# Optimization experiments

Measured on AMD Instinct MI355X. Metric: run time of the kernel, lower is better.

Reference implementation:

```python
import jax, jax.numpy as jnp
import numpy as np

NUM_HEADS = 8
OUT_DIM = 128
DEPTH = OUT_DIM // NUM_HEADS  # 16


def setup_inputs() -> dict:
    key = jax.random.key(0)
    ks = jax.random.split(key, 6)
    B, N, F_IN = 32, 512, 64
    x = jax.random.normal(ks[0], (B, N, F_IN), dtype=jnp.float32)
    adj = jax.random.uniform(ks[1], (B, N, N), dtype=jnp.float32)
    wq = jax.random.normal(ks[2], (F_IN, OUT_DIM), dtype=jnp.float32) * 0.05
    wk = jax.random.normal(ks[3], (F_IN, OUT_DIM), dtype=jnp.float32) * 0.05
    wv = jax.random.normal(ks[4], (F_IN, OUT_DIM), dtype=jnp.float32) * 0.05
    wo = jax.random.normal(ks[5], (OUT_DIM, OUT_DIM), dtype=jnp.float32) * 0.05
    return {"x": x, "adj": adj, "wq": wq, "wk": wk, "wv": wv, "wo": wo}


def _split_heads(t, B, N):
    # [B, N, out_dim] -> [B, H, N, D]
    return t.reshape(B, N, NUM_HEADS, DEPTH).transpose(0, 2, 1, 3)


def reference(x, adj, wq, wk, wv, wo):
    B, N, _ = x.shape
    q = _split_heads(x @ wq, B, N)  # [B,H,N,D]
    k = _split_heads(x @ wk, B, N)
    v = _split_heads(x @ wv, B, N)
    scale = jnp.sqrt(jnp.float32(DEPTH))
    scores = jnp.einsum("bhnd,bhmd->bhnm", q, k) / scale  # [B,H,N,N]
    attn = jnp.tanh(scores * adj[:, None, :, :])  # mask-multiply + tanh
    h = jnp.einsum("bhnm,bhmd->bhnd", attn, v)  # [B,H,N,D]
    h = h.transpose(0, 2, 1, 3).reshape(B, N, OUT_DIM)
    return jax.nn.relu(h @ wo)
```

## Files before the change

### kernel.cpp

```cpp
#include <hip/hip_runtime.h>


typedef __bf16 bf16x8 __attribute__((ext_vector_type(8)));
typedef __bf16 bf16x4 __attribute__((ext_vector_type(4)));
typedef float  f32x4  __attribute__((ext_vector_type(4)));

#define B_    32
#define N_    512
#define FIN_  64
#define H_    8
#define D_    16
#define OD_   128
#define BH_   (B_ * H_)

__global__ __launch_bounds__(256) void qkv_kernel(
    const float* __restrict__ x,  const float* __restrict__ wq,
    const float* __restrict__ wk, const float* __restrict__ wv,
    __bf16* __restrict__ Qb, __bf16* __restrict__ Kb, __bf16* __restrict__ VT)
{
    __shared__ __align__(16) __bf16 WT[384 * 72];

    const int tid = threadIdx.x;
    for (int idx = tid; idx < 384 * 64; idx += 256) {
        int j = idx % 384;
        int k = idx / 384;
        const float* w = (j < 128) ? wq : ((j < 256) ? wk : wv);
        int jj = j & 127;
        WT[j * 72 + k] = (__bf16)w[k * 128 + jj];
    }
    __syncthreads();

    const int lane = tid & 63;
    const int wv_id = tid >> 6;
    const int g    = lane >> 4;
    const int lr   = lane & 15;

    const int rowA = blockIdx.x * 64 + wv_id * 16 + lr;
    bf16x8 afrag[2];
#pragma unroll
    for (int kk = 0; kk < 2; ++kk) {
        const float* xp = x + rowA * 64 + kk * 32 + g * 8;
        f32x4 x0 = *(const f32x4*)(xp);
        f32x4 x1 = *(const f32x4*)(xp + 4);
        bf16x8 a;
#pragma unroll
        for (int e = 0; e < 4; ++e) { a[e] = (__bf16)x0[e]; a[4 + e] = (__bf16)x1[e]; }
        afrag[kk] = a;
    }

    const int b    = (blockIdx.x * 64) >> 9;
    const int nn0  = (blockIdx.x * 64 + wv_id * 16 + g * 4) & 511;

#pragma unroll 1
    for (int j0 = 0; j0 < 384; j0 += 16) {
        f32x4 acc = {0.f, 0.f, 0.f, 0.f};
#pragma unroll
        for (int kk = 0; kk < 2; ++kk) {
            bf16x8 bfrag = *(const bf16x8*)&WT[(j0 + lr) * 72 + kk * 32 + g * 8];
            acc = __builtin_amdgcn_mfma_f32_16x16x32_bf16(afrag[kk], bfrag, acc, 0, 0, 0);
        }
        const int t  = j0 >> 7;
        const int jj = (j0 + lr) & 127;
        const int h  = jj >> 4;
        const int d  = jj & 15;
        const int bh = b * 8 + h;
        if (t == 2) {
            bf16x4 pk;
#pragma unroll
            for (int r = 0; r < 4; ++r) pk[r] = (__bf16)acc[r];
            *(bf16x4*)&VT[(bh * 16 + d) * 512 + nn0] = pk;
        } else {
            __bf16* dst = (t == 0) ? Qb : Kb;
#pragma unroll
            for (int r = 0; r < 4; ++r)
                dst[(bh * 512 + (nn0 + r)) * 16 + d] = (__bf16)acc[r];
        }
    }
}

__device__ __forceinline__ float tanh_q(float sadj) {
    const float C = 0.7213475204444817f;
    float e = __builtin_amdgcn_exp2f(sadj * C);
    float r = __builtin_amdgcn_rcpf(e + 1.0f);
    return 1.0f - 2.0f * r;
}

__global__ __launch_bounds__(512) void attn_kernel(
    const float* __restrict__ adj,
    const __bf16* __restrict__ Qb, const __bf16* __restrict__ Kb,
    const __bf16* __restrict__ VT, __bf16* __restrict__ Hb)
{
    __shared__ __align__(16) __bf16 P[8][16][40];

    const int tid  = threadIdx.x;
    const int lane = tid & 63;
    const int h    = tid >> 6;
    const int g    = lane >> 4;
    const int lr   = lane & 15;
    const int b    = blockIdx.y;
    const int n0   = blockIdx.x * 16;
    const int bh   = b * 8 + h;

    bf16x8 qf = {};
    if (g < 2) qf = *(const bf16x8*)&Qb[(bh * 512 + n0 + lr) * 16 + g * 8];

    const float* adj_row = adj + ((long)b * 512 + n0 + lr) * 512;

    f32x4 accH = {0.f, 0.f, 0.f, 0.f};

    for (int m0 = 0; m0 < 512; m0 += 32) {
        bf16x8 kf0 = {}, kf1 = {};
        if (g < 2) {
            kf0 = *(const bf16x8*)&Kb[(bh * 512 + m0 +      lr) * 16 + g * 8];
            kf1 = *(const bf16x8*)&Kb[(bh * 512 + m0 + 16 + lr) * 16 + g * 8];
        }
        bf16x8 vf = *(const bf16x8*)&VT[(bh * 16 + lr) * 512 + m0 + g * 8];
        f32x4 a0 = *(const f32x4*)(adj_row + m0 +      g * 4);
        f32x4 a1 = *(const f32x4*)(adj_row + m0 + 16 + g * 4);

        const f32x4 z = {0.f, 0.f, 0.f, 0.f};
        f32x4 s0 = __builtin_amdgcn_mfma_f32_16x16x32_bf16(kf0, qf, z, 0, 0, 0);
        f32x4 s1 = __builtin_amdgcn_mfma_f32_16x16x32_bf16(kf1, qf, z, 0, 0, 0);

        bf16x4 p0, p1;
#pragma unroll
        for (int r = 0; r < 4; ++r) {
            p0[r] = (__bf16)tanh_q(s0[r] * a0[r]);
            p1[r] = (__bf16)tanh_q(s1[r] * a1[r]);
        }
        *(bf16x4*)&P[h][lr][g * 4]      = p0;
        *(bf16x4*)&P[h][lr][16 + g * 4] = p1;
        bf16x8 af = *(const bf16x8*)&P[h][lr][g * 8];

        accH = __builtin_amdgcn_mfma_f32_16x16x32_bf16(af, vf, accH, 0, 0, 0);
    }

#pragma unroll
    for (int r = 0; r < 4; ++r)
        Hb[((long)b * 512 + n0 + g * 4 + r) * 128 + h * 16 + lr] = (__bf16)accH[r];
}

__global__ __launch_bounds__(256) void oproj_kernel(
    const __bf16* __restrict__ Hb, const float* __restrict__ wo,
    float* __restrict__ out)
{
    __shared__ __align__(16) __bf16 WoT[128 * 136];

    const int tid = threadIdx.x;
    for (int idx = tid; idx < 128 * 128; idx += 256) {
        int j = idx & 127;
        int k = idx >> 7;
        WoT[j * 136 + k] = (__bf16)wo[k * 128 + j];
    }
    __syncthreads();

    const int lane = tid & 63;
    const int wv_id = tid >> 6;
    const int g    = lane >> 4;
    const int lr   = lane & 15;

    const int rowA = blockIdx.x * 64 + wv_id * 16 + lr;
    bf16x8 afrag[4];
#pragma unroll
    for (int kk = 0; kk < 4; ++kk)
        afrag[kk] = *(const bf16x8*)&Hb[(long)rowA * 128 + kk * 32 + g * 8];

    const int orow = blockIdx.x * 64 + wv_id * 16 + g * 4;
#pragma unroll 1
    for (int j0 = 0; j0 < 128; j0 += 16) {
        f32x4 acc = {0.f, 0.f, 0.f, 0.f};
#pragma unroll
        for (int kk = 0; kk < 4; ++kk) {
            bf16x8 bfrag = *(const bf16x8*)&WoT[(j0 + lr) * 136 + kk * 32 + g * 8];
            acc = __builtin_amdgcn_mfma_f32_16x16x32_bf16(afrag[kk], bfrag, acc, 0, 0, 0);
        }
#pragma unroll
        for (int r = 0; r < 4; ++r)
            out[(long)(orow + r) * 128 + j0 + lr] = fmaxf(acc[r], 0.0f);
    }
}

extern "C" void kernel_launch(void* const* d_in, const int* in_sizes, int n_in,
                              void* d_out, int out_size, void* d_ws, size_t ws_size,
                              hipStream_t stream) {
    const float* x   = (const float*)d_in[0];
    const float* adj = (const float*)d_in[1];
    const float* wq  = (const float*)d_in[2];
    const float* wk  = (const float*)d_in[3];
    const float* wv  = (const float*)d_in[4];
    const float* wo  = (const float*)d_in[5];
    float* out = (float*)d_out;

    __bf16* Qb = (__bf16*)d_ws;
    __bf16* Kb = Qb + BH_ * N_ * D_;
    __bf16* VT = Kb + BH_ * N_ * D_;
    __bf16* Hb = VT + BH_ * N_ * D_;

    qkv_kernel<<<256, 256, 0, stream>>>(x, wq, wk, wv, Qb, Kb, VT);
    attn_kernel<<<dim3(32, 32), 512, 0, stream>>>(adj, Qb, Kb, VT, Hb);
    oproj_kernel<<<256, 256, 0, stream>>>(Hb, wo, out);
}
```

Before: 153.9 us.

## Pre-transpose weights once, stage adj strip in LDS, drop P round-trip

Adds a prep kernel that converts and transposes the weights to bf16 once, so the qkv and oproj blocks no longer each rebuild a transposed weight copy in shared memory. Those blocks now cover 16 rows each, with the waves splitting the output columns, and launch four times as many blocks. The attention kernel loads the block's 16x512 adj strip cooperatively into swizzled shared memory with coalesced loads, and feeds the tanh result straight into the PV MFMA by reordering V loads, removing the per-iteration LDS write/read of P. Costs are an extra kernel launch and 32KB of shared memory per attention block, which may lower occupancy.

```diff
diff --git a/kernel.cpp b/kernel.cpp
--- a/kernel.cpp
+++ b/kernel.cpp
@@ -5,75 +5,71 @@
 typedef __bf16 bf16x4 __attribute__((ext_vector_type(4)));
 typedef float  f32x4  __attribute__((ext_vector_type(4)));
 
-#define B_    32
-#define N_    512
-#define FIN_  64
-#define H_    8
-#define D_    16
-#define OD_   128
-#define BH_   (B_ * H_)
+#define MFMA16(a, b, c) __builtin_amdgcn_mfma_f32_16x16x32_bf16((a), (b), (c), 0, 0, 0)
+
+__global__ __launch_bounds__(256) void prep_kernel(
+    const float* __restrict__ wq, const float* __restrict__ wk,
+    const float* __restrict__ wv, const float* __restrict__ wo,
+    __bf16* __restrict__ WTb, __bf16* __restrict__ WoTb)
+{
+    int idx = blockIdx.x * 256 + threadIdx.x;
+    if (idx < 6144) {
+        int j4 = idx % 96, k = idx / 96, j = j4 * 4;
+        const float* w = (j < 128) ? wq : ((j < 256) ? wk : wv);
+        f32x4 v = *(const f32x4*)&w[k * 128 + (j & 127)];
+#pragma unroll
+        for (int e = 0; e < 4; ++e) WTb[(j + e) * 64 + k] = (__bf16)v[e];
+    } else if (idx < 6144 + 4096) {
+        int i2 = idx - 6144;
+        int j4 = i2 % 32, k = i2 / 32, j = j4 * 4;
+        f32x4 v = *(const f32x4*)&wo[k * 128 + j];
+#pragma unroll
+        for (int e = 0; e < 4; ++e) WoTb[(j + e) * 128 + k] = (__bf16)v[e];
+    }
+}
 
 __global__ __launch_bounds__(256) void qkv_kernel(
-    const float* __restrict__ x,  const float* __restrict__ wq,
-    const float* __restrict__ wk, const float* __restrict__ wv,
+    const float* __restrict__ x, const __bf16* __restrict__ WTb,
     __bf16* __restrict__ Qb, __bf16* __restrict__ Kb, __bf16* __restrict__ VT)
 {
-    __shared__ __align__(16) __bf16 WT[384 * 72];
-
-    const int tid = threadIdx.x;
-    for (int idx = tid; idx < 384 * 64; idx += 256) {
-        int j = idx % 384;
-        int k = idx / 384;
-        const float* w = (j < 128) ? wq : ((j < 256) ? wk : wv);
-        int jj = j & 127;
-        WT[j * 72 + k] = (__bf16)w[k * 128 + jj];
-    }
-    __syncthreads();
-
-    const int lane = tid & 63;
-    const int wv_id = tid >> 6;
-    const int g    = lane >> 4;
-    const int lr   = lane & 15;
-
-    const int rowA = blockIdx.x * 64 + wv_id * 16 + lr;
-    bf16x8 afrag[2];
+    const int tid = threadIdx.x, lane = tid & 63, w = tid >> 6;
+    const int g = lane >> 4, lr = lane & 15;
+    const long R0 = (long)blockIdx.x * 16;
+    const int b = (int)(R0 >> 9);
+    const int nloc = (int)(R0 & 511) + g * 4;
+
+    bf16x8 af[2];
 #pragma unroll
     for (int kk = 0; kk < 2; ++kk) {
-        const float* xp = x + rowA * 64 + kk * 32 + g * 8;
-        f32x4 x0 = *(const f32x4*)(xp);
-        f32x4 x1 = *(const f32x4*)(xp + 4);
+        const float* xp = x + (R0 + lr) * 64 + kk * 32 + g * 8;
+        f32x4 x0 = *(const f32x4*)xp, x1 = *(const f32x4*)(xp + 4);
         bf16x8 a;
 #pragma unroll
         for (int e = 0; e < 4; ++e) { a[e] = (__bf16)x0[e]; a[4 + e] = (__bf16)x1[e]; }
-        afrag[kk] = a;
-    }
-
-    const int b    = (blockIdx.x * 64) >> 9;
-    const int nn0  = (blockIdx.x * 64 + wv_id * 16 + g * 4) & 511;
-
-#pragma unroll 1
-    for (int j0 = 0; j0 < 384; j0 += 16) {
+        af[kk] = a;
+    }
+
+#pragma unroll 2
+    for (int i = 0; i < 6; ++i) {
+        const int j0 = (w * 6 + i) * 16;
         f32x4 acc = {0.f, 0.f, 0.f, 0.f};
 #pragma unroll
         for (int kk = 0; kk < 2; ++kk) {
-            bf16x8 bfrag = *(const bf16x8*)&WT[(j0 + lr) * 72 + kk * 32 + g * 8];
-            acc = __builtin_amdgcn_mfma_f32_16x16x32_bf16(afrag[kk], bfrag, acc, 0, 0, 0);
-        }
-        const int t  = j0 >> 7;
-        const int jj = (j0 + lr) & 127;
-        const int h  = jj >> 4;
-        const int d  = jj & 15;
-        const int bh = b * 8 + h;
+            bf16x8 bf = *(const bf16x8*)&WTb[(j0 + lr) * 64 + kk * 32 + g * 8];
+            acc = MFMA16(af[kk], bf, acc);
+        }
+        const int jj = (j0 + lr) & 127, hh = jj >> 4, d = jj & 15;
+        const int bh = b * 8 + hh, t = j0 >> 7;
         if (t == 2) {
             bf16x4 pk;
 #pragma unroll
             for (int r = 0; r < 4; ++r) pk[r] = (__bf16)acc[r];
-            *(bf16x4*)&VT[(bh * 16 + d) * 512 + nn0] = pk;
+            *(bf16x4*)&VT[((long)bh * 16 + d) * 512 + nloc] = pk;
         } else {
-            __bf16* dst = (t == 0) ? Qb : Kb;
+            __bf16* dst = t ? Kb : Qb;
 #pragma unroll
             for (int r = 0; r < 4; ++r)
-                dst[(bh * 512 + (nn0 + r)) * 16 + d] = (__bf16)acc[r];
+                dst[((long)bh * 512 + nloc + r) * 16 + d] = (__bf16)acc[r];
         }
     }
 }
@@ -81,8 +77,7 @@
 __device__ __forceinline__ float tanh_q(float sadj) {
     const float C = 0.7213475204444817f;
     float e = __builtin_amdgcn_exp2f(sadj * C);
-    float r = __builtin_amdgcn_rcpf(e + 1.0f);
-    return 1.0f - 2.0f * r;
+    return 1.0f - 2.0f * __builtin_amdgcn_rcpf(e + 1.0f);
 }
 
 __global__ __launch_bounds__(512) void attn_kernel(
@@ -90,7 +85,7 @@
     const __bf16* __restrict__ Qb, const __bf16* __restrict__ Kb,
     const __bf16* __restrict__ VT, __bf16* __restrict__ Hb)
 {
-    __shared__ __align__(16) __bf16 P[8][16][40];
+    __shared__ __align__(16) float adjL[16][512];
 
     const int tid  = threadIdx.x;
     const int lane = tid & 63;
@@ -101,38 +96,55 @@
     const int n0   = blockIdx.x * 16;
     const int bh   = b * 8 + h;
 
+    const char* strip = (const char*)(adj + ((long)b * 512 + n0) * 512);
+    f32x4 tmp[4];
+#pragma unroll
+    for (int i = 0; i < 4; ++i)
+        tmp[i] = *(const f32x4*)(strip + i * 8192 + tid * 16);
+#pragma unroll
+    for (int i = 0; i < 4; ++i) {
+        int o = i * 8192 + tid * 16;
+        int row = o >> 11, col = o & 2047;
+        *(f32x4*)((char*)adjL + row * 2048 + (col ^ ((row & 7) << 4))) = tmp[i];
+    }
+
     bf16x8 qf = {};
-    if (g < 2) qf = *(const bf16x8*)&Qb[(bh * 512 + n0 + lr) * 16 + g * 8];
-
-    const float* adj_row = adj + ((long)b * 512 + n0 + lr) * 512;
+    if (g < 2) qf = *(const bf16x8*)&Qb[((long)bh * 512 + n0 + lr) * 16 + g * 8];
+
+    const __bf16* Kbase = Kb + (long)bh * 512 * 16;
+    const __bf16* Vrow  = VT + ((long)bh * 16 + lr) * 512;
+    const char*   aRow  = (const char*)adjL + lr * 2048;
+    const int     sw    = (lr & 7) << 4;
+
+    __syncthreads();
 
     f32x4 accH = {0.f, 0.f, 0.f, 0.f};
-
-    for (int m0 = 0; m0 < 512; m0 += 32) {
+#pragma unroll 2
+    for (int t = 0; t < 16; ++t) {
+        const int m0 = t * 32;
         bf16x8 kf0 = {}, kf1 = {};
         if (g < 2) {
-            kf0 = *(const bf16x8*)&Kb[(bh * 512 + m0 +      lr) * 16 + g * 8];
-            kf1 = *(const bf16x8*)&Kb[(bh * 512 + m0 + 16 + lr) * 16 + g * 8];
-        }
-        bf16x8 vf = *(const bf16x8*)&VT[(bh * 16 + lr) * 512 + m0 + g * 8];
-        f32x4 a0 = *(const f32x4*)(adj_row + m0 +      g * 4);
-        f32x4 a1 = *(const f32x4*)(adj_row + m0 + 16 + g * 4);
+            kf0 = *(const bf16x8*)&Kbase[(m0 + lr) * 16 + g * 8];
+            kf1 = *(const bf16x8*)&Kbase[(m0 + 16 + lr) * 16 + g * 8];
+        }
+        bf16x4 v0 = *(const bf16x4*)&Vrow[m0 + g * 4];
+        bf16x4 v1 = *(const bf16x4*)&Vrow[m0 + 16 + g * 4];
+        f32x4 a0 = *(const f32x4*)(aRow + (((m0 + g * 4) * 4) ^ sw));
+        f32x4 a1 = *(const f32x4*)(aRow + (((m0 + 16 + g * 4) * 4) ^ sw));
 
         const f32x4 z = {0.f, 0.f, 0.f, 0.f};
-        f32x4 s0 = __builtin_amdgcn_mfma_f32_16x16x32_bf16(kf0, qf, z, 0, 0, 0);
-        f32x4 s1 = __builtin_amdgcn_mfma_f32_16x16x32_bf16(kf1, qf, z, 0, 0, 0);
-
-        bf16x4 p0, p1;
+        f32x4 s0 = MFMA16(kf0, qf, z);
+        f32x4 s1 = MFMA16(kf1, qf, z);
+
+        bf16x8 paf, vf;
 #pragma unroll
         for (int r = 0; r < 4; ++r) {
-            p0[r] = (__bf16)tanh_q(s0[r] * a0[r]);
-            p1[r] = (__bf16)tanh_q(s1[r] * a1[r]);
-        }
-        *(bf16x4*)&P[h][lr][g * 4]      = p0;
-        *(bf16x4*)&P[h][lr][16 + g * 4] = p1;
-        bf16x8 af = *(const bf16x8*)&P[h][lr][g * 8];
-
-        accH = __builtin_amdgcn_mfma_f32_16x16x32_bf16(af, vf, accH, 0, 0, 0);
+            paf[r]     = (__bf16)tanh_q(s0[r] * a0[r]);
+            paf[4 + r] = (__bf16)tanh_q(s1[r] * a1[r]);
+            vf[r]      = v0[r];
+            vf[4 + r]  = v1[r];
+        }
+        accH = MFMA16(paf, vf, accH);
     }
 
 #pragma unroll
@@ -141,42 +153,30 @@
 }
 
 __global__ __launch_bounds__(256) void oproj_kernel(
-    const __bf16* __restrict__ Hb, const float* __restrict__ wo,
+    const __bf16* __restrict__ Hb, const __bf16* __restrict__ WoTb,
     float* __restrict__ out)
 {
-    __shared__ __align__(16) __bf16 WoT[128 * 136];
-
-    const int tid = threadIdx.x;
-    for (int idx = tid; idx < 128 * 128; idx += 256) {
-        int j = idx & 127;
-        int k = idx >> 7;
-        WoT[j * 136 + k] = (__bf16)wo[k * 128 + j];
-    }
-    __syncthreads();
-
-    const int lane = tid & 63;
-    const int wv_id = tid >> 6;
-    const int g    = lane >> 4;
-    const int lr   = lane & 15;
-
-    const int rowA = blockIdx.x * 64 + wv_id * 16 + lr;
-    bf16x8 afrag[4];
+    const int tid = threadIdx.x, lane = tid & 63, w = tid >> 6;
+    const int g = lane >> 4, lr = lane & 15;
+    const long R0 = (long)blockIdx.x * 16;
+
+    bf16x8 af[4];
 #pragma unroll
     for (int kk = 0; kk < 4; ++kk)
-        afrag[kk] = *(const bf16x8*)&Hb[(long)rowA * 128 + kk * 32 + g * 8];
-
-    const int orow = blockIdx.x * 64 + wv_id * 16 + g * 4;
-#pragma unroll 1
-    for (int j0 = 0; j0 < 128; j0 += 16) {
+        af[kk] = *(const bf16x8*)&Hb[(R0 + lr) * 128 + kk * 32 + g * 8];
+
+#pragma unroll
+    for (int i = 0; i < 2; ++i) {
+        const int j0 = w * 32 + i * 16;
         f32x4 acc = {0.f, 0.f, 0.f, 0.f};
 #pragma unroll
         for (int kk = 0; kk < 4; ++kk) {
-            bf16x8 bfrag = *(const bf16x8*)&WoT[(j0 + lr) * 136 + kk * 32 + g * 8];
-            acc = __builtin_amdgcn_mfma_f32_16x16x32_bf16(afrag[kk], bfrag, acc, 0, 0, 0);
+            bf16x8 bf = *(const bf16x8*)&WoTb[(j0 + lr) * 128 + kk * 32 + g * 8];
+            acc = MFMA16(af[kk], bf, acc);
         }
 #pragma unroll
         for (int r = 0; r < 4; ++r)
-            out[(long)(orow + r) * 128 + j0 + lr] = fmaxf(acc[r], 0.0f);
+            out[(R0 + g * 4 + r) * 128 + j0 + lr] = fmaxf(acc[r], 0.f);
     }
 }
 
@@ -191,12 +191,16 @@
     const float* wo  = (const float*)d_in[5];
     float* out = (float*)d_out;
 
-    __bf16* Qb = (__bf16*)d_ws;
-    __bf16* Kb = Qb + BH_ * N_ * D_;
-    __bf16* VT = Kb + BH_ * N_ * D_;
-    __bf16* Hb = VT + BH_ * N_ * D_;
-
-    qkv_kernel<<<256, 256, 0, stream>>>(x, wq, wk, wv, Qb, Kb, VT);
+    char* wsb = (char*)d_ws;
+    __bf16* WTb  = (__bf16*)wsb;
+    __bf16* WoTb = (__bf16*)(wsb + 49152);
+    __bf16* Qb   = (__bf16*)(wsb + 81920);
+    __bf16* Kb   = Qb + 2097152;
+    __bf16* VT   = Kb + 2097152;
+    __bf16* Hb   = VT + 2097152;
+
+    prep_kernel<<<40, 256, 0, stream>>>(wq, wk, wv, wo, WTb, WoTb);
+    qkv_kernel<<<1024, 256, 0, stream>>>(x, WTb, Qb, Kb, VT);
     attn_kernel<<<dim3(32, 32), 512, 0, stream>>>(adj, Qb, Kb, VT, Hb);
-    oproj_kernel<<<256, 256, 0, stream>>>(Hb, wo, out);
-}
+    oproj_kernel<<<1024, 256, 0, stream>>>(Hb, WoTb, out);
+}
```

Result: faster. 143.1 us (-7.0%).
